# Kernel tuning notes

Hardware: AMD Instinct MI355X
Metric: run time of the kernel (lower is better)

The kernel has to match this reference:

```python
import jax, jax.numpy as jnp
import numpy as np
import math

D_MODEL = 1024
N_HEADS = 16
D_K = D_MODEL // N_HEADS
THRESH = 0.1  # attention probs below this are zeroed


def setup_inputs() -> dict:
    key = jax.random.key(0)
    ks = jax.random.split(key, 9)
    B, S, D = 2, 2048, D_MODEL
    scale = 1.0 / math.sqrt(D)
    x = jax.random.normal(ks[0], (B, S, D), dtype=jnp.float32)
    Wq = jax.random.normal(ks[1], (D, D), dtype=jnp.float32) * scale
    bq = jax.random.normal(ks[2], (D,), dtype=jnp.float32) * 0.01
    Wk = jax.random.normal(ks[3], (D, D), dtype=jnp.float32) * scale
    bk = jax.random.normal(ks[4], (D,), dtype=jnp.float32) * 0.01
    Wv = jax.random.normal(ks[5], (D, D), dtype=jnp.float32) * scale
    bv = jax.random.normal(ks[6], (D,), dtype=jnp.float32) * 0.01
    Wo = jax.random.normal(ks[7], (D, D), dtype=jnp.float32) * scale
    bo = jax.random.normal(ks[8], (D,), dtype=jnp.float32) * 0.01
    return {"x": x, "Wq": Wq, "bq": bq, "Wk": Wk, "bk": bk,
            "Wv": Wv, "bv": bv, "Wo": Wo, "bo": bo}


def _split_heads(t):
    B, S, D = t.shape
    return t.reshape(B, S, N_HEADS, D_K).transpose(0, 2, 1, 3)  # [B,H,S,dk]


def reference(x, Wq, bq, Wk, bk, Wv, bv, Wo, bo):
    # torch nn.Linear: y = x @ W.T + b
    q = _split_heads(x @ Wq.T + bq)
    k = _split_heads(x @ Wk.T + bk)
    v = _split_heads(x @ Wv.T + bv)
    scores = jnp.einsum('bhqd,bhkd->bhqk', q, k) / math.sqrt(D_K)
    probs = jax.nn.softmax(scores, axis=-1)          # full unmasked softmax (returned)
    keep = probs >= THRESH                            # ~low_attention_mask
    probs_model = jnp.where(keep, probs, 0.0)        # masked_fill; dropout is identity in eval
    ctx = jnp.einsum('bhqk,bhkd->bhqd', probs_model, v)
    B, H, S, dk = ctx.shape
    merged = ctx.transpose(0, 2, 1, 3).reshape(B, S, H * dk)
    out = merged @ Wo.T + bo
    attention_sum = probs.sum(axis=1)                # [B,S,S] sum over heads
    attention_mask = keep.astype(jnp.float32).sum(axis=1)  # [B,S,S]
    return (out, attention_sum, attention_mask)
```

## Files before the change

### kernel.cpp

```cpp
#include <hip/hip_runtime.h>

#define SDIM 2048
#define DDIM 1024
#define NH 16
#define DK 64
#define NB 2
#define MROWS (NB * SDIM)
#define MAXEV 65536
#define EXPC 0.18033688011112f
#define L01 -3.3219281f

typedef _Float16 f16x8 __attribute__((ext_vector_type(8)));
typedef _Float16 f16x4 __attribute__((ext_vector_type(4)));
typedef float f32x4 __attribute__((ext_vector_type(4)));

__device__ __forceinline__ void ld_lds16(const _Float16* g, _Float16* l) {
  __builtin_amdgcn_global_load_lds(
      (const __attribute__((address_space(1))) void*)g,
      (__attribute__((address_space(3))) void*)l, 16, 0, 0);
}

__global__ __launch_bounds__(256) void cvt_f16(
    const float* __restrict__ x, const float* __restrict__ wq,
    const float* __restrict__ wk, const float* __restrict__ wv,
    _Float16* __restrict__ xh, _Float16* __restrict__ wqh,
    _Float16* __restrict__ wkh, _Float16* __restrict__ wvh) {
  int i = blockIdx.x * 256 + threadIdx.x;
  const float* src;
  _Float16* dst;
  int off;
  if (i < 1048576) {
    src = x; dst = xh; off = i;
  } else if (i < 1310720) {
    src = wq; dst = wqh; off = i - 1048576;
  } else if (i < 1572864) {
    src = wk; dst = wkh; off = i - 1310720;
  } else {
    src = wv; dst = wvh; off = i - 1572864;
  }
  float4 v = ((const float4*)src)[off];
  f16x4 h;
  h[0] = (_Float16)v.x; h[1] = (_Float16)v.y;
  h[2] = (_Float16)v.z; h[3] = (_Float16)v.w;
  ((f16x4*)dst)[off] = h;
}

__global__ __launch_bounds__(256, 2) void proj_gemm(
    const _Float16* __restrict__ xh, const _Float16* __restrict__ Wqh,
    const _Float16* __restrict__ Wkh, const _Float16* __restrict__ Wvh,
    const float* __restrict__ bq, const float* __restrict__ bk,
    const float* __restrict__ bv, _Float16* __restrict__ Qo,
    _Float16* __restrict__ Ko, float* __restrict__ Vo) {
  __shared__ _Float16 sA[128 * 64];
  __shared__ _Float16 sB[128 * 64];
  const int t = threadIdx.x;
  const int lane = t & 63, wv = t >> 6;
  const int lr = lane & 15, quad = lane >> 4;
  const int wm = wv >> 1, wn = wv & 1;
  const int m0 = blockIdx.y * 128, n0 = blockIdx.x * 128;
  const int z = blockIdx.z;
  const _Float16* Bp = z == 0 ? Wqh : (z == 1 ? Wkh : Wvh);
  const float* bias = z == 0 ? bq : (z == 1 ? bk : bv);

  const int strow = t >> 3;
  const int stchunk = t & 7;
  const int stsrc = (stchunk ^ (strow & 7)) * 8;

  f32x4 acc[4][4];
#pragma unroll
  for (int i = 0; i < 4; ++i)
#pragma unroll
    for (int j = 0; j < 4; ++j) acc[i][j] = (f32x4){0.f, 0.f, 0.f, 0.f};

  for (int k0 = 0; k0 < DDIM; k0 += 64) {
    __syncthreads();
#pragma unroll
    for (int i = 0; i < 4; ++i) {
      const int row = i * 32 + strow;
      ld_lds16(&xh[(size_t)(m0 + row) * DDIM + k0 + stsrc],
               &sA[row * 64 + stchunk * 8]);
      ld_lds16(&Bp[(size_t)(n0 + row) * DDIM + k0 + stsrc],
               &sB[row * 64 + stchunk * 8]);
    }
    __syncthreads();
    f16x8 af[4][2], bf[4][2];
#pragma unroll
    for (int i = 0; i < 4; ++i)
#pragma unroll
      for (int kk = 0; kk < 2; ++kk) {
        const int ph = ((kk * 4 + quad) ^ (lr & 7)) * 8;
        af[i][kk] = *(const f16x8*)&sA[(wm * 64 + i * 16 + lr) * 64 + ph];
        bf[i][kk] = *(const f16x8*)&sB[(wn * 64 + i * 16 + lr) * 64 + ph];
      }
#pragma unroll
    for (int kk = 0; kk < 2; ++kk)
#pragma unroll
      for (int i = 0; i < 4; ++i)
#pragma unroll
        for (int j = 0; j < 4; ++j)
          acc[i][j] = __builtin_amdgcn_mfma_f32_16x16x32_f16(
              af[i][kk], bf[j][kk], acc[i][j], 0, 0, 0);
  }
#pragma unroll
  for (int j = 0; j < 4; ++j) {
    const int ng = n0 + wn * 64 + j * 16 + lr;
    const float bvv = bias[ng];
    const int h = ng >> 6, d = ng & 63;
#pragma unroll
    for (int i = 0; i < 4; ++i) {
#pragma unroll
      for (int r = 0; r < 4; ++r) {
        const int mg = m0 + wm * 64 + i * 16 + quad * 4 + r;
        const int b = mg >> 11, s = mg & 2047;
        const float o = acc[i][j][r] + bvv;
        const size_t off = ((size_t)(b * NH + h) * SDIM + s) * DK + d;
        if (z == 0)
          Qo[off] = (_Float16)(o * EXPC);
        else if (z == 1)
          Ko[off] = (_Float16)o;
        else
          Vo[off] = o;
      }
    }
  }
}

__global__ __launch_bounds__(256, 8) void attn_denom(
    const _Float16* __restrict__ Q, const _Float16* __restrict__ K,
    float* __restrict__ laOut) {
  __shared__ _Float16 KdA[64 * 64];
  __shared__ _Float16 KdB[64 * 64];
  const int t = threadIdx.x;
  const int lane = t & 63, wave = t >> 6;
  const int quad = lane >> 4, lr = lane & 15;
  const int q0 = blockIdx.x * 64;
  const int bh = blockIdx.y;
  const _Float16* Qh = Q + (size_t)bh * SDIM * DK;
  const _Float16* Kh = K + (size_t)bh * SDIM * DK;
  const size_t qoff = (size_t)(q0 + wave * 16 + lr) * DK + quad * 8;
  const f16x8 aq0 = *(const f16x8*)&Qh[qoff];
  const f16x8 aq1 = *(const f16x8*)&Qh[qoff + 32];
  const int strow = t >> 3, stchunk = t & 7;
  const int stsrc = (stchunk ^ (strow & 7)) * 8;
  const int ph0 = (quad ^ (lr & 7)) * 8;
  const int ph1 = ((4 + quad) ^ (lr & 7)) * 8;

#define STAGE_DN(KT, BUF)                                                  \
  {                                                                        \
    _Pragma("unroll") for (int i = 0; i < 2; ++i)                          \
        ld_lds16(&Kh[(size_t)((KT)*64 + i * 32 + strow) * DK + stsrc],     \
                 &BUF[(i * 32 + strow) * 64 + stchunk * 8]);               \
  }

#define COMPUTE_DN(BUF)                                                   \
  _Pragma("unroll") for (int c = 0; c < 4; ++c) {                         \
    f16x8 b0 = *(const f16x8*)&BUF[(c * 16 + lr) * 64 + ph0];             \
    f16x8 b1 = *(const f16x8*)&BUF[(c * 16 + lr) * 64 + ph1];             \
    f32x4 acc = {0.f, 0.f, 0.f, 0.f};                                     \
    acc = __builtin_amdgcn_mfma_f32_16x16x32_f16(aq0, b0, acc, 0, 0, 0);  \
    acc = __builtin_amdgcn_mfma_f32_16x16x32_f16(aq1, b1, acc, 0, 0, 0);  \
    _Pragma("unroll") for (int r = 0; r < 4; ++r)                         \
        dsum[r] += __builtin_amdgcn_exp2f(acc[r]);                        \
  }

  float dsum[4] = {0.f, 0.f, 0.f, 0.f};
  STAGE_DN(0, KdA);
#pragma unroll 1
  for (int kt = 0; kt < 32; kt += 2) {
    __syncthreads();
    STAGE_DN(kt + 1, KdB);
    COMPUTE_DN(KdA);
    __syncthreads();
    if (kt + 2 < 32) STAGE_DN(kt + 2, KdA);
    COMPUTE_DN(KdB);
  }
#pragma unroll
  for (int m = 1; m < 16; m <<= 1)
#pragma unroll
    for (int r = 0; r < 4; ++r)
      dsum[r] += __shfl_xor(dsum[r], m, 64);
  if (lr == 0) {
#pragma unroll
    for (int r = 0; r < 4; ++r)
      laOut[(size_t)bh * SDIM + q0 + wave * 16 + quad * 4 + r] =
          -__builtin_amdgcn_logf(dsum[r]);
  }
#undef STAGE_DN
#undef COMPUTE_DN
}

__global__ __launch_bounds__(256, 6) void attn_pass2(
    const _Float16* __restrict__ Q, const _Float16* __restrict__ K,
    const float* __restrict__ la, float* __restrict__ attSum,
    float* __restrict__ attMask, float4* __restrict__ ev,
    int* __restrict__ ecnt) {
  __shared__ __align__(16) float SMEM[64 * 68];
  _Float16* KbufA = (_Float16*)SMEM;
  _Float16* KbufB = (_Float16*)SMEM + 4096;
  float* Tbuf = SMEM;
  const int t = threadIdx.x;
  const int lane = t & 63, wave = t >> 6;
  const int quad = lane >> 4, lr = lane & 15;
  const int k0 = blockIdx.x * 64;
  const int q0 = blockIdx.y * 64;
  const int b = blockIdx.z;
  const int strow = t >> 3, stchunk = t & 7;
  const int stsrc = (stchunk ^ (strow & 7)) * 8;
  const int ph0 = (quad ^ (lr & 7)) * 8;
  const int ph1 = ((4 + quad) ^ (lr & 7)) * 8;

  const size_t qbase = ((size_t)(b * NH) * SDIM + q0 + wave * 16 + lr) * DK;
  const size_t dbase = (size_t)(b * NH) * SDIM + q0 + wave * 16 + quad * 4;
  const size_t hstep = (size_t)SDIM * DK;

  float asum[4][4] = {};
  float amask[4][4] = {};
  float mxr[4] = {-1e30f, -1e30f, -1e30f, -1e30f};

  f16x8 aq0c, aq1c, aq0n, aq1n;
  float4 lavc, lavn;

#define STAGE_H(H, BUF)                                                      \
  {                                                                          \
    const _Float16* Kp =                                                     \
        K + (size_t)(b * NH + (H)) * hstep + (size_t)k0 * DK;                \
    _Pragma("unroll") for (int i = 0; i < 2; ++i)                            \
        ld_lds16(&Kp[(size_t)(i * 32 + strow) * DK + stsrc],                 \
                 &BUF[(i * 32 + strow) * 64 + stchunk * 8]);                 \
  }

#define LOADQ_H(H, A0, A1, LV)                                               \
  {                                                                          \
    const size_t ho = (size_t)(H)*hstep;                                     \
    A0 = *(const f16x8*)&Q[qbase + ho + quad * 8];                           \
    A1 = *(const f16x8*)&Q[qbase + ho + 32 + quad * 8];                      \
    LV = *(const float4*)&la[dbase + (size_t)(H)*SDIM];                      \
  }

#define COMPUTE_H(BUF, A0, A1, LV)                                           \
  {                                                                          \
    const float lar[4] = {LV.x, LV.y, LV.z, LV.w};                           \
    _Pragma("unroll") for (int c = 0; c < 4; ++c) {                          \
      f16x8 b0 = *(const f16x8*)&BUF[(c * 16 + lr) * 64 + ph0];              \
      f16x8 b1 = *(const f16x8*)&BUF[(c * 16 + lr) * 64 + ph1];              \
      f32x4 acc = {0.f, 0.f, 0.f, 0.f};                                      \
      acc = __builtin_amdgcn_mfma_f32_16x16x32_f16(A0, b0, acc, 0, 0, 0);    \
      acc = __builtin_amdgcn_mfma_f32_16x16x32_f16(A1, b1, acc, 0, 0, 0);    \
      _Pragma("unroll") for (int r = 0; r < 4; ++r) {                        \
        const float arg = acc[r] + lar[r];                                   \
        mxr[r] = fmaxf(mxr[r], arg);                                         \
        asum[c][r] += __builtin_amdgcn_exp2f(arg);                           \
      }                                                                      \
    }                                                                        \
  }

  STAGE_H(0, KbufA);
  LOADQ_H(0, aq0c, aq1c, lavc);
#pragma unroll 1
  for (int h = 0; h < NH; h += 2) {
    __syncthreads();
    STAGE_H(h + 1, KbufB);
    LOADQ_H(h + 1, aq0n, aq1n, lavn);
    COMPUTE_H(KbufA, aq0c, aq1c, lavc);
    __syncthreads();
    if (h + 2 < NH) {
      STAGE_H(h + 2, KbufA);
      LOADQ_H(h + 2, aq0c, aq1c, lavc);
    }
    COMPUTE_H(KbufB, aq0n, aq1n, lavn);
  }
#undef STAGE_H
#undef LOADQ_H
#undef COMPUTE_H

  const float mx =
      fmaxf(fmaxf(mxr[0], mxr[1]), fmaxf(mxr[2], mxr[3]));
  if (__any(mx >= L01)) {
#pragma unroll 1
    for (int h = 0; h < NH; ++h) {
      const _Float16* Kp =
          K + (size_t)(b * NH + h) * hstep + (size_t)k0 * DK;
      const size_t ho = (size_t)h * hstep;
      const f16x8 aq0 = *(const f16x8*)&Q[qbase + ho + quad * 8];
      const f16x8 aq1 = *(const f16x8*)&Q[qbase + ho + 32 + quad * 8];
      const float4 l4 = *(const float4*)&la[dbase + (size_t)h * SDIM];
      const float lar[4] = {l4.x, l4.y, l4.z, l4.w};
#pragma unroll 1
      for (int c = 0; c < 4; ++c) {
        const f16x8 b0 = *(const f16x8*)&Kp[(c * 16 + lr) * DK + quad * 8];
        const f16x8 b1 = *(const f16x8*)&Kp[(c * 16 + lr) * DK + 32 + quad * 8];
        f32x4 acc = {0.f, 0.f, 0.f, 0.f};
        acc = __builtin_amdgcn_mfma_f32_16x16x32_f16(aq0, b0, acc, 0, 0, 0);
        acc = __builtin_amdgcn_mfma_f32_16x16x32_f16(aq1, b1, acc, 0, 0, 0);
#pragma unroll 1
        for (int r = 0; r < 4; ++r) {
          const float p = __builtin_amdgcn_exp2f(acc[r] + lar[r]);
          if (p >= 0.1f) {
            amask[c][r] += 1.0f;
            int idx = atomicAdd(ecnt, 1);
            if (idx < MAXEV)
              ev[idx] = make_float4(
                  __int_as_float(b * NH + h),
                  __int_as_float(q0 + wave * 16 + quad * 4 + r),
                  __int_as_float(k0 + c * 16 + lr), p);
          }
        }
      }
    }
  }
  const int g8 = t >> 3;
  const int l8 = (t & 7) * 4;
  __syncthreads();
#pragma unroll
  for (int c = 0; c < 4; ++c)
#pragma unroll
    for (int r = 0; r < 4; ++r)
      Tbuf[(wave * 16 + quad * 4 + r) * 68 + c * 16 + lr] = asum[c][r];
  __syncthreads();
#pragma unroll
  for (int p = 0; p < 2; ++p)
#pragma unroll
    for (int qh = 0; qh < 2; ++qh) {
      const int row = p * 32 + g8, col = qh * 32 + l8;
      f32x4 v = *(const f32x4*)&Tbuf[row * 68 + col];
      __builtin_nontemporal_store(
          v, (f32x4*)&attSum[((size_t)(b * SDIM) + q0 + row) * SDIM + k0 + col]);
    }
  __syncthreads();
#pragma unroll
  for (int c = 0; c < 4; ++c)
#pragma unroll
    for (int r = 0; r < 4; ++r)
      Tbuf[(wave * 16 + quad * 4 + r) * 68 + c * 16 + lr] = amask[c][r];
  __syncthreads();
#pragma unroll
  for (int p = 0; p < 2; ++p)
#pragma unroll
    for (int qh = 0; qh < 2; ++qh) {
      const int row = p * 32 + g8, col = qh * 32 + l8;
      f32x4 v = *(const f32x4*)&Tbuf[row * 68 + col];
      __builtin_nontemporal_store(
          v,
          (f32x4*)&attMask[((size_t)(b * SDIM) + q0 + row) * SDIM + k0 + col]);
    }
}

__global__ __launch_bounds__(64) void apply_events(
    const float4* __restrict__ ev, const int* __restrict__ ecnt,
    const float* __restrict__ V, float* __restrict__ merged,
    int* __restrict__ flags) {
  int n = *ecnt;
  if (n > MAXEV) n = MAXEV;
  const int d = threadIdx.x;
  for (int e = blockIdx.x; e < n; e += gridDim.x) {
    float4 r = ev[e];
    int bh = __float_as_int(r.x);
    int q = __float_as_int(r.y);
    int kc = __float_as_int(r.z);
    float p = r.w;
    int b = bh >> 4, h = bh & 15;
    atomicAdd(&merged[((size_t)(b * SDIM + q)) * DDIM + h * DK + d],
              p * V[((size_t)bh * SDIM + kc) * DK + d]);
    if (d == 0) flags[b * SDIM + q] = 1;
  }
}

__global__ __launch_bounds__(256) void out_gemm(const float* __restrict__ A,
                                                const float* __restrict__ W,
                                                const float* __restrict__ bias,
                                                float* __restrict__ out,
                                                const int* __restrict__ flags) {
  __shared__ float As[16][68];
  __shared__ float Ws[16][68];
  __shared__ int anyF;
  const int t = threadIdx.x;
  const int tx = t & 15, ty = t >> 4;
  const int m0 = blockIdx.y * 64;
  const int n0 = blockIdx.x * 64;
  if (t == 0) anyF = 0;
  __syncthreads();
  if (t < 64 && flags[m0 + t]) anyF = 1;
  __syncthreads();
  const int nb = n0 + tx * 4;
  const float4 bv = *(const float4*)&bias[nb];
  if (!anyF) {
#pragma unroll
    for (int r = 0; r < 4; ++r)
      *(float4*)&out[(size_t)(m0 + ty * 4 + r) * DDIM + nb] = bv;
    return;
  }
  const int lr = t >> 2;
  const int lc = (t & 3) * 4;
  float acc[4][4] = {};
  for (int k0 = 0; k0 < DDIM; k0 += 16) {
    __syncthreads();
    float4 av = *(const float4*)&A[(size_t)(m0 + lr) * DDIM + k0 + lc];
    float4 wv = *(const float4*)&W[(size_t)(n0 + lr) * DDIM + k0 + lc];
    As[lc + 0][lr] = av.x; As[lc + 1][lr] = av.y;
    As[lc + 2][lr] = av.z; As[lc + 3][lr] = av.w;
    Ws[lc + 0][lr] = wv.x; Ws[lc + 1][lr] = wv.y;
    Ws[lc + 2][lr] = wv.z; Ws[lc + 3][lr] = wv.w;
    __syncthreads();
#pragma unroll
    for (int kk = 0; kk < 16; ++kk) {
      float4 a4 = *(const float4*)&As[kk][ty * 4];
      float4 b4 = *(const float4*)&Ws[kk][tx * 4];
      const float a[4] = {a4.x, a4.y, a4.z, a4.w};
      const float b[4] = {b4.x, b4.y, b4.z, b4.w};
#pragma unroll
      for (int r = 0; r < 4; ++r)
#pragma unroll
        for (int c = 0; c < 4; ++c)
          acc[r][c] = fmaf(a[r], b[c], acc[r][c]);
    }
  }
#pragma unroll
  for (int r = 0; r < 4; ++r) {
    float4 o;
    o.x = acc[r][0] + bv.x;
    o.y = acc[r][1] + bv.y;
    o.z = acc[r][2] + bv.z;
    o.w = acc[r][3] + bv.w;
    *(float4*)&out[(size_t)(m0 + ty * 4 + r) * DDIM + nb] = o;
  }
}

extern "C" void kernel_launch(void* const* d_in, const int* in_sizes, int n_in,
                              void* d_out, int out_size, void* d_ws,
                              size_t ws_size, hipStream_t stream) {
  const float* x = (const float*)d_in[0];
  const float* Wq = (const float*)d_in[1];
  const float* bq = (const float*)d_in[2];
  const float* Wk = (const float*)d_in[3];
  const float* bk = (const float*)d_in[4];
  const float* Wv = (const float*)d_in[5];
  const float* bv = (const float*)d_in[6];
  const float* Wo = (const float*)d_in[7];
  const float* bo = (const float*)d_in[8];

  float* out = (float*)d_out;
  float* attSum = out + (size_t)MROWS * DDIM;
  float* attMask = attSum + (size_t)NB * SDIM * SDIM;

  char* ws = (char*)d_ws;
  const size_t bigF = (size_t)MROWS * DDIM * sizeof(float);
  const size_t bigH = (size_t)MROWS * DDIM * sizeof(_Float16);
  const size_t wH = (size_t)DDIM * DDIM * sizeof(_Float16);
  _Float16* Qh = (_Float16*)ws;  ws += bigH;
  _Float16* Kh = (_Float16*)ws;  ws += bigH;
  float* V = (float*)ws;         ws += bigF;
  float* merged = (float*)ws;    ws += bigF;
  _Float16* xh = (_Float16*)ws;  ws += bigH;
  _Float16* Wqh = (_Float16*)ws; ws += wH;
  _Float16* Wkh = (_Float16*)ws; ws += wH;
  _Float16* Wvh = (_Float16*)ws; ws += wH;
  float* laBuf = (float*)ws;     ws += (size_t)NB * NH * SDIM * sizeof(float);
  float4* ev = (float4*)ws;      ws += (size_t)MAXEV * sizeof(float4);
  int* flags = (int*)ws;         ws += (size_t)MROWS * sizeof(int);
  int* ecnt = (int*)ws;          ws += 16;

  hipMemsetAsync(merged, 0, bigF, stream);
  hipMemsetAsync(flags, 0, (size_t)MROWS * sizeof(int), stream);
  hipMemsetAsync(ecnt, 0, 16, stream);

  dim3 blk(256);
  cvt_f16<<<dim3(7168), blk, 0, stream>>>(x, Wq, Wk, Wv, xh, Wqh, Wkh, Wvh);
  proj_gemm<<<dim3(8, 32, 3), blk, 0, stream>>>(xh, Wqh, Wkh, Wvh, bq, bk, bv,
                                                Qh, Kh, V);
  attn_denom<<<dim3(32, 32), blk, 0, stream>>>(Qh, Kh, laBuf);
  attn_pass2<<<dim3(32, 32, 2), blk, 0, stream>>>(Qh, Kh, laBuf, attSum,
                                                  attMask, ev, ecnt);
  apply_events<<<dim3(256), dim3(64), 0, stream>>>(ev, ecnt, V, merged, flags);
  out_gemm<<<dim3(16, 64), blk, 0, stream>>>(merged, Wo, bo, out, flags);
}
```

Baseline: 297.3 us.

## Swizzle attention grids per XCD and write sparse mask via memset

```diff
diff --git a/kernel.cpp b/kernel.cpp
--- a/kernel.cpp
+++ b/kernel.cpp
@@ -133,8 +133,10 @@
   const int t = threadIdx.x;
   const int lane = t & 63, wave = t >> 6;
   const int quad = lane >> 4, lr = lane & 15;
-  const int q0 = blockIdx.x * 64;
-  const int bh = blockIdx.y;
+  const int id = blockIdx.x;
+  const int xcd = id & 7, inner = id >> 3;
+  const int bh = xcd * 4 + (inner >> 5);
+  const int q0 = (inner & 31) * 64;
   const _Float16* Qh = Q + (size_t)bh * SDIM * DK;
   const _Float16* Kh = K + (size_t)bh * SDIM * DK;
   const size_t qoff = (size_t)(q0 + wave * 16 + lr) * DK + quad * 8;
@@ -201,9 +203,11 @@
   const int t = threadIdx.x;
   const int lane = t & 63, wave = t >> 6;
   const int quad = lane >> 4, lr = lane & 15;
-  const int k0 = blockIdx.x * 64;
-  const int q0 = blockIdx.y * 64;
-  const int b = blockIdx.z;
+  const int id = blockIdx.x;
+  const int xcd = id & 7, inner = id >> 3;
+  const int b = xcd >> 2;
+  const int q0 = (((xcd >> 1) & 1) * 16 + (inner >> 4)) * 64;
+  const int k0 = ((xcd & 1) * 16 + (inner & 15)) * 64;
   const int strow = t >> 3, stchunk = t & 7;
   const int stsrc = (stchunk ^ (strow & 7)) * 8;
   const int ph0 = (quad ^ (lr & 7)) * 8;
@@ -214,7 +218,6 @@
   const size_t hstep = (size_t)SDIM * DK;
 
   float asum[4][4] = {};
-  float amask[4][4] = {};
   float mxr[4] = {-1e30f, -1e30f, -1e30f, -1e30f};
 
   f16x8 aq0c, aq1c, aq0n, aq1n;
@@ -276,6 +279,7 @@
   const float mx =
       fmaxf(fmaxf(mxr[0], mxr[1]), fmaxf(mxr[2], mxr[3]));
   if (__any(mx >= L01)) {
+    float amask[4][4] = {};
 #pragma unroll 1
     for (int h = 0; h < NH; ++h) {
       const _Float16* Kp =
@@ -307,6 +311,14 @@
         }
       }
     }
+#pragma unroll
+    for (int c = 0; c < 4; ++c)
+#pragma unroll
+      for (int r = 0; r < 4; ++r)
+        if (amask[c][r] != 0.0f) {
+          const size_t row = (size_t)(b * SDIM) + q0 + wave * 16 + quad * 4 + r;
+          attMask[row * SDIM + k0 + c * 16 + lr] = amask[c][r];
+        }
   }
   const int g8 = t >> 3;
   const int l8 = (t & 7) * 4;
@@ -325,23 +337,6 @@
       f32x4 v = *(const f32x4*)&Tbuf[row * 68 + col];
       __builtin_nontemporal_store(
           v, (f32x4*)&attSum[((size_t)(b * SDIM) + q0 + row) * SDIM + k0 + col]);
-    }
-  __syncthreads();
-#pragma unroll
-  for (int c = 0; c < 4; ++c)
-#pragma unroll
-    for (int r = 0; r < 4; ++r)
-      Tbuf[(wave * 16 + quad * 4 + r) * 68 + c * 16 + lr] = amask[c][r];
-  __syncthreads();
-#pragma unroll
-  for (int p = 0; p < 2; ++p)
-#pragma unroll
-    for (int qh = 0; qh < 2; ++qh) {
-      const int row = p * 32 + g8, col = qh * 32 + l8;
-      f32x4 v = *(const f32x4*)&Tbuf[row * 68 + col];
-      __builtin_nontemporal_store(
-          v,
-          (f32x4*)&attMask[((size_t)(b * SDIM) + q0 + row) * SDIM + k0 + col]);
     }
 }
 
@@ -462,14 +457,15 @@
   hipMemsetAsync(merged, 0, bigF, stream);
   hipMemsetAsync(flags, 0, (size_t)MROWS * sizeof(int), stream);
   hipMemsetAsync(ecnt, 0, 16, stream);
+  hipMemsetAsync(attMask, 0, (size_t)NB * SDIM * SDIM * sizeof(float), stream);
 
   dim3 blk(256);
   cvt_f16<<<dim3(7168), blk, 0, stream>>>(x, Wq, Wk, Wv, xh, Wqh, Wkh, Wvh);
   proj_gemm<<<dim3(8, 32, 3), blk, 0, stream>>>(xh, Wqh, Wkh, Wvh, bq, bk, bv,
                                                 Qh, Kh, V);
-  attn_denom<<<dim3(32, 32), blk, 0, stream>>>(Qh, Kh, laBuf);
-  attn_pass2<<<dim3(32, 32, 2), blk, 0, stream>>>(Qh, Kh, laBuf, attSum,
-                                                  attMask, ev, ecnt);
+  attn_denom<<<dim3(1024), blk, 0, stream>>>(Qh, Kh, laBuf);
+  attn_pass2<<<dim3(2048), blk, 0, stream>>>(Qh, Kh, laBuf, attSum,
+                                             attMask, ev, ecnt);
   apply_events<<<dim3(256), dim3(64), 0, stream>>>(ev, ecnt, V, merged, flags);
   out_gemm<<<dim3(16, 64), blk, 0, stream>>>(merged, Wo, bo, out, flags);
 }
```

New measurement: 267.8 us. 9.9% less time.
